# Kernel tuning notes

Hardware: AMD Instinct MI355X
Metric: run time of the kernel (lower is better)

The kernel has to match this reference:

```python
import jax, jax.numpy as jnp
import numpy as np

NUM_FRAMES = 24
FRAME_SIZE = 8          # heads per frame; attention_probs.shape[0] = NUM_FRAMES*FRAME_SIZE
DIM_X = 32
DIM_Y = 32
SEQ = 300
STRENGTHEN_SCALE = 0.125
WEAKEN_SCALE = 0.918
INJECTION_SCALE = 1.0
KERNEL_DIVISION = 3.0
LEN_PROMPT = 8          # 'A basketball player missing a three-point shot'
TRAILING = 100
# token_inds=[2,3] union trailing range (9..108); order irrelevant (uniform write)
TOKEN_INDS = np.array(sorted(set([2, 3]) | set(range(LEN_PROMPT + 1, LEN_PROMPT + TRAILING + 1))), dtype=np.int32)
_LEFTS = [0.05, 0.0717, 0.0935, 0.1152, 0.137, 0.1587, 0.1804, 0.2022, 0.2239, 0.2457,
          0.2674, 0.2891, 0.3109, 0.3326, 0.3543, 0.3761, 0.3978, 0.4196, 0.4413, 0.463,
          0.4848, 0.5065, 0.5283, 0.55]
# [top, left, bottom, right] ratios per frame (matches init_kwargs bbox_per_frame)
BBOX_PER_FRAME = [(0.25, l, 0.75, round(l + 0.3, 4)) for l in _LEFTS]


def _bbox_px(ratios, dim_x, dim_y):
    top = int(dim_y * ratios[0]); left = int(dim_x * ratios[1])
    bottom = int(dim_y * ratios[2]); right = int(dim_x * ratios[3])
    return top, left, bottom, right


def _gauss_patch(h, w):
    # torch.linspace(0, h, h): h points, endpoint inclusive; mx=int(h/2), sx=h/3
    x = jnp.linspace(0.0, float(h), h)[:, None]
    y = jnp.linspace(0.0, float(w), w)[None, :]
    sx, sy = h / KERNEL_DIVISION, w / KERNEL_DIVISION
    g = jnp.exp(-(((x - h // 2) ** 2) / (2.0 * sx * sx) + ((y - w // 2) ** 2) / (2.0 * sy * sy)))
    return g / g.max()  # 1/(2*pi*sx*sy) prefactor cancels under max-normalization


def _forward(attention_probs, dim_x, dim_y):
    F = NUM_FRAMES
    fs = attention_probs.shape[0] // F
    seq = attention_probs.shape[-1]
    max_val = attention_probs.max()
    scale = max_val * INJECTION_SCALE
    # strengthen map is identical across heads-within-frame and across selected tokens:
    # build a compact [F, dim_y, dim_x] map instead of the full 4D zeros_like tensor.
    wm = jnp.zeros((F, dim_y, dim_x), attention_probs.dtype)
    for i, r in enumerate(BBOX_PER_FRAME):  # fixed small frame count, trace-time loop
        t, l, b, rt = _bbox_px(r, dim_x, dim_y)
        wm = wm.at[i, t:b, l:rt].set(_gauss_patch(b - t, rt - l).astype(attention_probs.dtype) * scale)
    inds = TOKEN_INDS
    ap5 = attention_probs.reshape(F, fs, dim_y, dim_x, seq)
    sel = ap5[..., inds]                     # [F, fs, dy, dx, T]
    wmb = wm[:, None, :, :, None]            # broadcast over heads & tokens
    weaken = jnp.where(wmb == 0, WEAKEN_SCALE, 1.0).astype(attention_probs.dtype)
    new_sel = sel * weaken + STRENGTHEN_SCALE * wmb
    out = ap5.at[..., inds].set(new_sel)
    return out.reshape(attention_probs.shape)


def setup_inputs() -> dict:
    key = jax.random.key(0)
    ap = jax.random.uniform(key, (NUM_FRAMES * FRAME_SIZE, DIM_Y, DIM_X, SEQ), dtype=jnp.float32)
    return {"attention_probs": ap, "dim_x": DIM_X, "dim_y": DIM_Y}


def reference(attention_probs, dim_x, dim_y):
    return _forward(attention_probs, dim_x, dim_y)
```

## Files before the change

### kernel.cpp

```cpp
#include <hip/hip_runtime.h>

#define SEQ        300
#define V4         (SEQ / 4)
#define NROWS      (192 * 32 * 32)
#define N4         (NROWS * V4)
#define NFRAMES    24
#define UNROLL     4
#define TTOT       (N4 / UNROLL)
#define P1BLOCKS   (TTOT / 256)
#define ROWSTEP    (TTOT / V4)
#define FSTEP      (ROWSTEP >> 13)

typedef float f32x4 __attribute__((ext_vector_type(4)));

__constant__ int c_left[NFRAMES]  = {1,2,2,3,4,5,5,6,7,7,8,9,9,10,11,12,12,13,14,14,15,16,16,17};
__constant__ int c_width[NFRAMES] = {10,9,10,10,9,9,10,10,9,10,10,9,10,10,9,9,10,10,9,10,10,9,10,10};

#define BB(l, w) ((((1u << (w)) - 1u) << (l)))
__constant__ unsigned c_bbox[NFRAMES] = {
    BB(1,10), BB(2,9),  BB(2,10), BB(3,10), BB(4,9),  BB(5,9),
    BB(5,10), BB(6,10), BB(7,9),  BB(7,10), BB(8,10), BB(9,9),
    BB(9,10), BB(10,10),BB(11,9), BB(12,9), BB(12,10),BB(13,10),
    BB(14,9), BB(14,10),BB(15,10),BB(16,9), BB(16,10),BB(17,10)
};

#define Wq 0.918f
#define W4 Wq,Wq,Wq,Wq,
#define O4 1.0f,1.0f,1.0f,1.0f,
__constant__ __align__(16) float c_wf[300] = {
    1.0f,1.0f,Wq,Wq,
    O4
    1.0f,Wq,Wq,Wq,
    W4 W4 W4 W4 W4 W4 W4 W4 W4 W4 W4 W4
    W4 W4 W4 W4 W4 W4 W4 W4 W4 W4 W4 W4
    Wq,1.0f,1.0f,1.0f,
    O4 O4 O4 O4 O4 O4 O4 O4 O4 O4 O4 O4
    O4 O4 O4 O4 O4 O4 O4 O4 O4 O4 O4 O4
    O4 O4 O4 O4 O4 O4 O4 O4 O4 O4 O4 O4
    O4 O4 O4 O4 O4 O4 O4 O4 O4 O4 O4
};

__device__ __forceinline__ float wave_max64(float v) {
    #pragma unroll
    for (int off = 32; off > 0; off >>= 1)
        v = fmaxf(v, __shfl_down(v, off, 64));
    return v;
}

__global__ void __launch_bounds__(256) kphase1(const f32x4* __restrict__ in,
                                               f32x4* __restrict__ out,
                                               float* __restrict__ bmax) {
    const int t    = blockIdx.x * 256 + threadIdx.x;
    const int row0 = t / V4;
    const int c    = t - row0 * V4;
    const int f0   = row0 >> 13;
    const int yy   = (row0 >> 5) & 31;
    const int xx   = row0 & 31;
    const bool yIn = (yy >= 8) & (yy < 24);
    const f32x4 wf = ((const f32x4*)c_wf)[c];

    f32x4 v[UNROLL];
    #pragma unroll
    for (int j = 0; j < UNROLL; j++)
        v[j] = __builtin_nontemporal_load(in + t + j * TTOT);

    float m = 0.0f;
    #pragma unroll
    for (int j = 0; j < UNROLL; j++) {
        f32x4 x = v[j];
        m = fmaxf(m, fmaxf(fmaxf(x[0], x[1]), fmaxf(x[2], x[3])));
        const bool inB = yIn && ((c_bbox[f0 + j * FSTEP] >> xx) & 1u);
        f32x4 r = inB ? x : (x * wf);
        out[t + j * TTOT] = r;
    }

    m = wave_max64(m);
    __shared__ float sw[4];
    const int lane = threadIdx.x & 63, wv = threadIdx.x >> 6;
    if (lane == 0) sw[wv] = m;
    __syncthreads();
    if (threadIdx.x == 0)
        bmax[blockIdx.x] = fmaxf(fmaxf(sw[0], sw[1]), fmaxf(sw[2], sw[3]));
}

__global__ void kwm(const float* __restrict__ bmax, float* __restrict__ wm) {
    __shared__ float patch[16 * 10];
    __shared__ float sw[4];
    __shared__ float s_scale, s_gmax;
    const int f = blockIdx.x;
    const int tid = threadIdx.x;

    float m = 0.0f;
    for (int i = tid; i < P1BLOCKS; i += 256) m = fmaxf(m, bmax[i]);
    m = wave_max64(m);
    if ((tid & 63) == 0) sw[tid >> 6] = m;
    __syncthreads();
    if (tid == 0) s_scale = fmaxf(fmaxf(sw[0], sw[1]), fmaxf(sw[2], sw[3]));

    const int w = c_width[f], l = c_left[f];
    if (tid < 16 * w) {
        int i = tid / w, j = tid - i * w;
        float x = (float)i * (16.0f / 15.0f);
        float y = (float)j * ((float)w / (float)(w - 1));
        float dx = x - 8.0f;
        float dy = y - (float)(w / 2);
        float sx = 16.0f / 3.0f;
        float sy = (float)w / 3.0f;
        patch[tid] = expf(-(dx * dx / (2.0f * sx * sx) + dy * dy / (2.0f * sy * sy)));
    }
    __syncthreads();
    if (tid == 0) {
        float g = 0.0f;
        for (int k = 0; k < 16 * w; k++) g = fmaxf(g, patch[k]);
        s_gmax = g;
    }
    __syncthreads();
    const float mul = s_scale / s_gmax;
    for (int p = tid; p < 1024; p += 256) {
        int yy = p >> 5, xx = p & 31;
        float v = 0.0f;
        if (yy >= 8 && yy < 24 && xx >= l && xx < l + w)
            v = patch[(yy - 8) * w + (xx - l)] * mul;
        wm[f * 1024 + p] = v;
    }
}

__global__ void kinject(float* __restrict__ out, const float* __restrict__ wm) {
    const int b  = blockIdx.x;
    const int f  = b >> 7;
    const int fs = (b >> 4) & 7;
    const int yy = (b & 15) + 8;
    const int l  = c_left[f], w = c_width[f];
    const int r0 = ((f * 8 + fs) * 32 + yy) * 32;
    const int total = w * 102;

    for (int t = threadIdx.x; t < total; t += 256) {
        int xi = t / 102;
        int si = t - xi * 102;
        int s  = (si < 2) ? (si + 2) : (si + 7);
        float add = 0.125f * wm[f * 1024 + yy * 32 + l + xi];
        out[(r0 + l + xi) * SEQ + s] += add;
    }
}

extern "C" void kernel_launch(void* const* d_in, const int* in_sizes, int n_in,
                              void* d_out, int out_size, void* d_ws, size_t ws_size,
                              hipStream_t stream) {
    const float* ap = (const float*)d_in[0];
    float* out = (float*)d_out;
    float* ws  = (float*)d_ws;
    float* bmax = ws;
    float* wm   = ws + P1BLOCKS;

    kphase1<<<P1BLOCKS, 256, 0, stream>>>((const f32x4*)ap, (f32x4*)out, bmax);
    kwm<<<NFRAMES, 256, 0, stream>>>(bmax, wm);
    kinject<<<24 * 8 * 16, 256, 0, stream>>>(out, wm);
}
```

Measured before the change: 408.0 us.

## Fuse weight-map build into inject kernel and use nontemporal stores

Removes the separate kwm kernel. Each inject block now reduces the per-block maxima itself and computes its Gaussian patch in shared memory, which cuts one launch and the intermediate weight-map buffer. In exchange, every one of the 3072 blocks repeats the bmax reduction and the patch computation. The phase-1 output stores are also made nontemporal to avoid cache pollution, at the risk that the later read-modify-write in kinject misses in cache.

```diff
diff --git a/kernel.cpp b/kernel.cpp
--- a/kernel.cpp
+++ b/kernel.cpp
@@ -71,7 +71,7 @@
         m = fmaxf(m, fmaxf(fmaxf(x[0], x[1]), fmaxf(x[2], x[3])));
         const bool inB = yIn && ((c_bbox[f0 + j * FSTEP] >> xx) & 1u);
         f32x4 r = inB ? x : (x * wf);
-        out[t + j * TTOT] = r;
+        __builtin_nontemporal_store(r, out + t + j * TTOT);
     }
 
     m = wave_max64(m);
@@ -83,21 +83,23 @@
         bmax[blockIdx.x] = fmaxf(fmaxf(sw[0], sw[1]), fmaxf(sw[2], sw[3]));
 }
 
-__global__ void kwm(const float* __restrict__ bmax, float* __restrict__ wm) {
+__global__ void __launch_bounds__(256) kinject(float* __restrict__ out,
+                                               const float* __restrict__ bmax) {
     __shared__ float patch[16 * 10];
     __shared__ float sw[4];
     __shared__ float s_scale, s_gmax;
-    const int f = blockIdx.x;
+    const int b   = blockIdx.x;
+    const int f   = b >> 7;
+    const int fs  = (b >> 4) & 7;
+    const int yy  = (b & 15) + 8;
     const int tid = threadIdx.x;
+    const int l   = c_left[f], w = c_width[f];
 
     float m = 0.0f;
     for (int i = tid; i < P1BLOCKS; i += 256) m = fmaxf(m, bmax[i]);
     m = wave_max64(m);
     if ((tid & 63) == 0) sw[tid >> 6] = m;
-    __syncthreads();
-    if (tid == 0) s_scale = fmaxf(fmaxf(sw[0], sw[1]), fmaxf(sw[2], sw[3]));
 
-    const int w = c_width[f], l = c_left[f];
     if (tid < 16 * w) {
         int i = tid / w, j = tid - i * w;
         float x = (float)i * (16.0f / 15.0f);
@@ -110,36 +112,23 @@
     }
     __syncthreads();
     if (tid == 0) {
+        s_scale = fmaxf(fmaxf(sw[0], sw[1]), fmaxf(sw[2], sw[3]));
         float g = 0.0f;
         for (int k = 0; k < 16 * w; k++) g = fmaxf(g, patch[k]);
         s_gmax = g;
     }
     __syncthreads();
-    const float mul = s_scale / s_gmax;
-    for (int p = tid; p < 1024; p += 256) {
-        int yy = p >> 5, xx = p & 31;
-        float v = 0.0f;
-        if (yy >= 8 && yy < 24 && xx >= l && xx < l + w)
-            v = patch[(yy - 8) * w + (xx - l)] * mul;
-        wm[f * 1024 + p] = v;
-    }
-}
 
-__global__ void kinject(float* __restrict__ out, const float* __restrict__ wm) {
-    const int b  = blockIdx.x;
-    const int f  = b >> 7;
-    const int fs = (b >> 4) & 7;
-    const int yy = (b & 15) + 8;
-    const int l  = c_left[f], w = c_width[f];
+    const float mul = 0.125f * s_scale / s_gmax;
     const int r0 = ((f * 8 + fs) * 32 + yy) * 32;
     const int total = w * 102;
+    const float* prow = &patch[(yy - 8) * w];
 
-    for (int t = threadIdx.x; t < total; t += 256) {
+    for (int t = tid; t < total; t += 256) {
         int xi = t / 102;
         int si = t - xi * 102;
         int s  = (si < 2) ? (si + 2) : (si + 7);
-        float add = 0.125f * wm[f * 1024 + yy * 32 + l + xi];
-        out[(r0 + l + xi) * SEQ + s] += add;
+        out[(r0 + l + xi) * SEQ + s] += mul * prow[xi];
     }
 }
 
@@ -150,9 +139,7 @@
     float* out = (float*)d_out;
     float* ws  = (float*)d_ws;
     float* bmax = ws;
-    float* wm   = ws + P1BLOCKS;
 
     kphase1<<<P1BLOCKS, 256, 0, stream>>>((const f32x4*)ap, (f32x4*)out, bmax);
-    kwm<<<NFRAMES, 256, 0, stream>>>(bmax, wm);
-    kinject<<<24 * 8 * 16, 256, 0, stream>>>(out, wm);
+    kinject<<<24 * 8 * 16, 256, 0, stream>>>(out, bmax);
 }
```

After: 420.8 us. 3.1% more time.
